# Kernel optimization log

Measured on AMD Instinct MI355X. Metric: run time of the kernel, lower is better.

Reference implementation:

```python
import jax, jax.numpy as jnp
import numpy as np

T = 1048576  # time-series length
INTERVAL_EPOCH = 10


def setup_inputs() -> dict:
    key = jax.random.key(0)
    x = jax.random.uniform(key, (T, 9), dtype=jnp.float32)
    p = lambda v: jnp.array([v], dtype=jnp.float32)
    return {
        "x": x,
        "f_0": p(0.9), "f_c": p(0.5), "k": p(0.2), "n": p(0.9),
        "d_p": p(0.0001), "evap": p(0.29), "evap_constant": p(0.02),
        "missing_restrict": p(2.0), "missing": p(0.2),
        "w_r_1": p(1.0), "w_r_2": p(1.0), "w_z_1": p(1.0), "w_z_2": p(1.0),
        "epoch": 20,
    }


def _runflow(x, f_0, f_c, k, n, d_p, evap, evap_constant,
             missing_restrict, missing, w_r_1, w_r_2, w_z_1, w_z_2, epoch):
    greenland  = x[:, 0]
    impervious = x[:, 2]
    area       = x[:, 3]
    slope      = x[:, 4]
    prec       = x[:, 6]
    total_prec = x[:, 7]
    area_id    = x[0, 8]

    f0, fc, k0, n0 = f_0[0], f_c[0], k[0], n[0]
    dp, ev, evc = d_p[0], evap[0], evap_constant[0]
    mr, miss = missing_restrict[0], missing[0]
    wr1, wr2, wz1, wz2 = w_r_1[0], w_r_2[0], w_z_1[0], w_z_2[0]

    # --- antecedent precipitation recurrence: prec_pre[i] depends on prec_pre[i-1], prec[i-1]
    pp0 = total_prec[0] - prec[0]

    def pp_step(carry, p_prev):
        last = jnp.where(carry > mr, mr + (carry - mr) * miss, carry)
        new = (last + p_prev) * (1.0 - ev) - evc
        return new, new

    _, pp_tail = jax.lax.scan(pp_step, pp0, prec[:-1])
    prec_pre = jax.nn.relu(jnp.concatenate([pp0[None], pp_tail]))  # [T]

    # --- Horton infiltration + rational/Manning runoff (elementwise)
    f_t = (f0 - fc) * jnp.exp(-(k0 * total_prec)) + fc
    q_greenland = jax.nn.relu(prec_pre / 1000.0 * (greenland * area) * (1.0 - f_t))
    d_imperv = jax.nn.relu(prec_pre / 1000.0 - dp)
    q_imperv = jax.nn.relu(jnp.sqrt(impervious * area) * (1.49 / n0)
                           * d_imperv ** (5.0 / 3.0) * jnp.sqrt(slope))
    q = q_imperv + q_greenland  # [T]

    # --- delay: special catchments (3723, 870) shift by 1 step, others by 4
    rid = jnp.round(area_id)
    shift = jnp.where((rid == 3723.0) | (rid == 870.0), 1, 4)
    idx = jnp.arange(T)
    q_shift = jnp.where(idx < shift, 0.0, q[(idx - shift) % T])  # zero-padded delay

    if epoch > INTERVAL_EPOCH:
        # --- linear RNN routing: h_i = h_{i-1}*wr1 + q_i*wr2 ; q2_i = h_i*wz1 + q_i*wz2
        def rt_step(h, qi):
            h_new = h * wr1 + qi * wr2
            return h_new, h_new * wz1 + qi * wz2

        _, q2_tail = jax.lax.scan(rt_step, jnp.float32(0.0), q_shift[1:])
        q2 = jnp.concatenate([q_shift[:1], q2_tail])
        return q2.reshape(T, 1, 1)
    return q_shift.reshape(T, 1, 1)


def reference(x, f_0, f_c, k, n, d_p, evap, evap_constant,
              missing_restrict, missing, w_r_1, w_r_2, w_z_1, w_z_2, epoch):
    return _runflow(x, f_0, f_c, k, n, d_p, evap, evap_constant,
                    missing_restrict, missing, w_r_1, w_r_2, w_z_1, w_z_2, epoch)
```

## Files before the change

kernel.cpp:

```cpp
#include <hip/hip_runtime.h>

#define T_N     1048576
#define BLK     256
#define S_OUT   8
#define R_BLOCK (BLK * S_OUT)
#define NB      (T_N / R_BLOCK)
#define NTH     (T_N / S_OUT)
#define WARM    64
#define HALO    (WARM + 4)
#define SW(u)   ((u) + ((u) >> 3))

__device__ __forceinline__ float pp_step(float c, float p, float mr, float miss,
                                         float omev, float evc) {
    float last = (c > mr) ? fmaf(c - mr, miss, mr) : c;
    return fmaf(last + p, omev, -evc);
}

__global__ __launch_bounds__(BLK) void k_main(
    const float* __restrict__ x,
    const float* __restrict__ f0p, const float* __restrict__ fcp,
    const float* __restrict__ kp,  const float* __restrict__ nnp,
    const float* __restrict__ dpp, const float* __restrict__ evp,
    const float* __restrict__ evcp,const float* __restrict__ mrp,
    const float* __restrict__ missp,
    const float* __restrict__ wr1p,const float* __restrict__ wr2p,
    const float* __restrict__ wz1p,const float* __restrict__ wz2p,
    const int*   __restrict__ epp,
    float* __restrict__ out, float* __restrict__ Bthr, float* __restrict__ Bblk)
{
    __shared__ float s_prec[SW(R_BLOCK + HALO - 1) + 1];
    __shared__ float s_cG[SW(R_BLOCK + 3) + 1];
    __shared__ float s_cA[SW(R_BLOCK + 3) + 1];
    __shared__ float s_B[BLK];

    const int b = blockIdx.x, t = threadIdx.x;
    const int row0 = b * R_BLOCK;

    const float f0 = *f0p, fc = *fcp, kk = *kp, nn = *nnp;
    const float dp = *dpp, ev = *evp, evc = *evcp, mr = *mrp, miss = *missp;
    const float wr1 = *wr1p, wr2 = *wr2p, wz1 = *wz1p, wz2 = *wz2p;
    const int ep = *epp;
    const float omev = 1.0f - ev;
    const float cimp = 1.49f / nn;
    const float f0mfc = f0 - fc;

    const float rid = rintf(x[8]);
    const int shift = (rid == 3723.0f || rid == 870.0f) ? 1 : 4;
    const float pp0 = x[7] - x[6];

    for (int u = t; u < R_BLOCK + HALO; u += BLK) {
        int r = row0 - HALO + u;
        s_prec[SW(u)] = (r >= 0) ? x[r * 9 + 6] : 0.0f;
    }
    for (int u = t; u < R_BLOCK + 4; u += BLK) {
        int r = row0 - 4 + u;
        float cg = 0.0f, ca = 0.0f;
        if (r >= 0) {
            const float* row = x + r * 9;
            float gl = row[0], imp = row[2], ar = row[3], sl = row[4], tp = row[7];
            float ft = fmaf(f0mfc, __expf(-kk * tp), fc);
            cg = gl * ar * (1.0f - ft) * 0.001f;
            ca = sqrtf(imp * ar) * cimp * sqrtf(sl);
        }
        s_cG[SW(u)] = cg;
        s_cA[SW(u)] = ca;
    }
    __syncthreads();

    const int i0 = row0 + t * S_OUT;
    const int rb = i0 - shift;
    int rr = rb - WARM; if (rr < 0) rr = 0;
    float c = (rr == 0) ? pp0 : 0.0f;
    const int rs = (rb < 0) ? 0 : rb;
    for (; rr < rs; ++rr)
        c = pp_step(c, s_prec[SW(rr - row0 + HALO)], mr, miss, omev, evc);

    float outl[S_OUT];
    float h = 0.0f;
    for (int j = 0; j < S_OUT; ++j) {
        const int i = i0 + j;
        const int r = i - shift;
        float qs = 0.0f;
        if (r >= 0) {
            float pre = fmaxf(c, 0.0f);
            int ci = r - row0 + 4;
            float qg = fmaxf(pre * s_cG[SW(ci)], 0.0f);
            float di = fmaxf(fmaf(pre, 0.001f, -dp), 0.0f);
            float qi = fmaxf(s_cA[SW(ci)] * __powf(di, 5.0f / 3.0f), 0.0f);
            qs = qg + qi;
            c = pp_step(c, s_prec[SW(r - row0 + HALO)], mr, miss, omev, evc);
        }
        h = fmaf(wr1, h, wr2 * qs);
        outl[j] = (ep > 10) ? fmaf(wz1, h, wz2 * qs) : qs;
    }

    float4* op = reinterpret_cast<float4*>(out + i0);
    op[0] = make_float4(outl[0], outl[1], outl[2], outl[3]);
    op[1] = make_float4(outl[4], outl[5], outl[6], outl[7]);

    float Bv = (ep > 10) ? h : 0.0f;
    s_B[t] = Bv;
    Bthr[b * BLK + t] = Bv;
    __syncthreads();
    if (t == 0) {
        const float at = powf(wr1, (float)S_OUT);
        float acc = 0.0f;
        for (int u = 0; u < BLK; ++u) acc = fmaf(at, acc, s_B[u]);
        Bblk[b] = acc;
    }
}

__global__ __launch_bounds__(BLK) void k_fix(
    float* __restrict__ out,
    const float* __restrict__ Bthr, const float* __restrict__ Bblk,
    const float* __restrict__ wr1p, const float* __restrict__ wz1p)
{
    __shared__ float sBb[NB];
    __shared__ float sB[BLK];
    __shared__ float carr[BLK];
    __shared__ float sred[BLK];
    const int b = blockIdx.x, t = threadIdx.x;
    const float wr1 = *wr1p, wz1 = *wz1p;
    for (int u = t; u < NB; u += BLK) sBb[u] = Bblk[u];
    sB[t] = Bthr[b * BLK + t];
    __syncthreads();

    const float ab = powf(wr1, (float)R_BLOCK);
    const float at = powf(wr1, (float)S_OUT);
    float partial = 0.0f;
    for (int u = t; u < b; u += BLK)
        partial = fmaf(sBb[u], powf(ab, (float)(b - 1 - u)), partial);
    sred[t] = partial;
    __syncthreads();
    for (int off = BLK / 2; off > 0; off >>= 1) {
        if (t < off) sred[t] += sred[t + off];
        __syncthreads();
    }
    if (t == 0) {
        float cth = sred[0];
        for (int u = 0; u < BLK; ++u) { carr[u] = cth; cth = fmaf(at, cth, sB[u]); }
    }
    __syncthreads();

    float hin = carr[t];
    if (hin != 0.0f) {
        float4* op = reinterpret_cast<float4*>(out + b * R_BLOCK + t * S_OUT);
        float4 v0 = op[0], v1 = op[1];
        float p = hin * wz1;
        p *= wr1; v0.x += p; p *= wr1; v0.y += p; p *= wr1; v0.z += p; p *= wr1; v0.w += p;
        p *= wr1; v1.x += p; p *= wr1; v1.y += p; p *= wr1; v1.z += p; p *= wr1; v1.w += p;
        op[0] = v0;
        op[1] = v1;
    }
}

extern "C" void kernel_launch(void* const* d_in, const int* in_sizes, int n_in,
                              void* d_out, int out_size, void* d_ws, size_t ws_size,
                              hipStream_t stream) {
    const float* x = (const float*)d_in[0];
    float* out  = (float*)d_out;
    float* Bthr = (float*)d_ws;
    float* Bblk = Bthr + NTH;

    k_main<<<NB, BLK, 0, stream>>>(x,
        (const float*)d_in[1],  (const float*)d_in[2],  (const float*)d_in[3],
        (const float*)d_in[4],  (const float*)d_in[5],  (const float*)d_in[6],
        (const float*)d_in[7],  (const float*)d_in[8],  (const float*)d_in[9],
        (const float*)d_in[10], (const float*)d_in[11], (const float*)d_in[12],
        (const float*)d_in[13], (const int*)d_in[14],
        out, Bthr, Bblk);

    k_fix<<<NB, BLK, 0, stream>>>(out, Bthr, Bblk,
        (const float*)d_in[10], (const float*)d_in[12]);
}
```

Baseline: 123.1 us.

## Stage x rows via coalesced float4 loads into column-split LDS

```diff
diff --git a/kernel.cpp b/kernel.cpp
--- a/kernel.cpp
+++ b/kernel.cpp
@@ -8,7 +8,14 @@
 #define NTH     (T_N / S_OUT)
 #define WARM    64
 #define HALO    (WARM + 4)
-#define SW(u)   ((u) + ((u) >> 3))
+#define NROWS   (R_BLOCK + HALO)
+#define NV      (NROWS * 9 / 4)
+#define LPAD    2384
+#define NCOL    6
+#define CID_PREC 4
+#define CID_TP   5
+#define COL_LUT 0xF54F321F0ull
+#define PA(lr)  ((lr) + ((lr) >> 3))
 
 __device__ __forceinline__ float pp_step(float c, float p, float mr, float miss,
                                          float omev, float evc) {
@@ -28,9 +35,7 @@
     const int*   __restrict__ epp,
     float* __restrict__ out, float* __restrict__ Bthr, float* __restrict__ Bblk)
 {
-    __shared__ float s_prec[SW(R_BLOCK + HALO - 1) + 1];
-    __shared__ float s_cG[SW(R_BLOCK + 3) + 1];
-    __shared__ float s_cA[SW(R_BLOCK + 3) + 1];
+    __shared__ float s_x[NCOL * LPAD];
     __shared__ float s_B[BLK];
 
     const int b = blockIdx.x, t = threadIdx.x;
@@ -48,22 +53,24 @@
     const int shift = (rid == 3723.0f || rid == 870.0f) ? 1 : 4;
     const float pp0 = x[7] - x[6];
 
-    for (int u = t; u < R_BLOCK + HALO; u += BLK) {
-        int r = row0 - HALO + u;
-        s_prec[SW(u)] = (r >= 0) ? x[r * 9 + 6] : 0.0f;
-    }
-    for (int u = t; u < R_BLOCK + 4; u += BLK) {
-        int r = row0 - 4 + u;
-        float cg = 0.0f, ca = 0.0f;
-        if (r >= 0) {
-            const float* row = x + r * 9;
-            float gl = row[0], imp = row[2], ar = row[3], sl = row[4], tp = row[7];
-            float ft = fmaf(f0mfc, __expf(-kk * tp), fc);
-            cg = gl * ar * (1.0f - ft) * 0.001f;
-            ca = sqrtf(imp * ar) * cimp * sqrtf(sl);
+    const int startf = (row0 - HALO) * 9;
+    for (int v = t; v < NV; v += BLK) {
+        int g = startf + 4 * v;
+        if (g >= 0) {
+            const float4 val = *reinterpret_cast<const float4*>(x + g);
+            unsigned ug = (unsigned)g;
+            int r   = (int)(ug / 9u);
+            int col = (int)(ug - 9u * (unsigned)r);
+            int lr  = r - row0 + HALO;
+            float fv[4] = {val.x, val.y, val.z, val.w};
+            #pragma unroll
+            for (int k = 0; k < 4; ++k) {
+                int cid = (int)((COL_LUT >> (4 * col)) & 0xFull);
+                if (cid < NCOL) s_x[cid * LPAD + PA(lr)] = fv[k];
+                col++;
+                if (col == 9) { col = 0; lr++; }
+            }
         }
-        s_cG[SW(u)] = cg;
-        s_cA[SW(u)] = ca;
     }
     __syncthreads();
 
@@ -71,24 +78,34 @@
     const int rb = i0 - shift;
     int rr = rb - WARM; if (rr < 0) rr = 0;
     float c = (rr == 0) ? pp0 : 0.0f;
-    const int rs = (rb < 0) ? 0 : rb;
-    for (; rr < rs; ++rr)
-        c = pp_step(c, s_prec[SW(rr - row0 + HALO)], mr, miss, omev, evc);
+    for (; rr < rb; ++rr) {
+        int lr = rr - row0 + HALO;
+        c = pp_step(c, s_x[CID_PREC * LPAD + PA(lr)], mr, miss, omev, evc);
+    }
 
     float outl[S_OUT];
     float h = 0.0f;
+    #pragma unroll
     for (int j = 0; j < S_OUT; ++j) {
-        const int i = i0 + j;
-        const int r = i - shift;
+        const int r = i0 + j - shift;
         float qs = 0.0f;
         if (r >= 0) {
+            int a = PA(r - row0 + HALO);
+            float gl = s_x[0 * LPAD + a];
+            float im = s_x[1 * LPAD + a];
+            float ar = s_x[2 * LPAD + a];
+            float sl = s_x[3 * LPAD + a];
+            float pr = s_x[CID_PREC * LPAD + a];
+            float tp = s_x[CID_TP   * LPAD + a];
             float pre = fmaxf(c, 0.0f);
-            int ci = r - row0 + 4;
-            float qg = fmaxf(pre * s_cG[SW(ci)], 0.0f);
+            float ft = fmaf(f0mfc, __expf(-kk * tp), fc);
+            float cg = gl * ar * (1.0f - ft) * 0.001f;
+            float ca = sqrtf(im * ar) * cimp * sqrtf(sl);
+            float qg = fmaxf(pre * cg, 0.0f);
             float di = fmaxf(fmaf(pre, 0.001f, -dp), 0.0f);
-            float qi = fmaxf(s_cA[SW(ci)] * __powf(di, 5.0f / 3.0f), 0.0f);
+            float qi = fmaxf(ca * __powf(di, 5.0f / 3.0f), 0.0f);
             qs = qg + qi;
-            c = pp_step(c, s_prec[SW(r - row0 + HALO)], mr, miss, omev, evc);
+            c = pp_step(c, pr, mr, miss, omev, evc);
         }
         h = fmaf(wr1, h, wr2 * qs);
         outl[j] = (ep > 10) ? fmaf(wz1, h, wz2 * qs) : qs;
```

Result: slower. 131.5 us (+6.8%).
